# Performance work log

Hardware: AMD Instinct MI355X
Metric: run time of the kernel (lower is better)

Reference implementation:

```python
import jax, jax.numpy as jnp
import numpy as np

N1, N2, E = 256, 128, 4096

def _conv(x, w, b):
    # NCHW conv, 3x3, padding=1 (SAME), then ReLU
    y = jax.lax.conv_general_dilated(x, w, (1, 1), 'SAME',
                                     dimension_numbers=('NCHW', 'OIHW', 'NCHW'))
    return jax.nn.relu(y + b[None, :, None, None])

def _pool(x):
    return jax.lax.reduce_window(x, -jnp.inf, jax.lax.max,
                                 (1, 1, 2, 2), (1, 1, 2, 2), 'VALID')

def _sage(x, src, dst, wl, bl, wr, n):
    # torch_geometric SAGEConv: out = lin_l(mean_j x_src) + lin_r(x), then L2 normalize
    agg = jax.ops.segment_sum(x[src], dst, num_segments=n)
    cnt = jax.ops.segment_sum(jnp.ones((src.shape[0],), x.dtype), dst, num_segments=n)
    agg = agg / jnp.maximum(cnt, 1.0)[:, None]
    out = agg @ wl.T + bl + x @ wr.T
    return out / jnp.maximum(jnp.linalg.norm(out, axis=-1, keepdims=True), 1e-12)

def _diff_pool(x, adj, s):
    # torch_geometric dense_diff_pool
    s = jax.nn.softmax(s, axis=-1)
    out = jnp.einsum('bnc,bnf->bcf', s, x)
    out_adj = jnp.einsum('bnc,bnm,bmd->bcd', s, adj, s)
    link = adj - jnp.einsum('bnc,bmc->bnm', s, s)
    link_loss = jnp.sqrt(jnp.sum(link * link)) / adj.size
    ent_loss = jnp.mean(jnp.sum(-s * jnp.log(s + 1e-15), axis=-1))
    return out, out_adj, link_loss, ent_loss

def setup_inputs() -> dict:
    key = jax.random.key(0)
    ks = jax.random.split(key, 16)
    rn = lambda k, shape, sc: jax.random.normal(k, shape, jnp.float32) * sc
    inp = {}
    inp['inputs'] = jax.random.normal(ks[0], (1, 5, 512, 512), jnp.float32)
    inp['edge_index'] = jax.random.randint(ks[1], (2, E), 0, N1)
    chans = [(5, 32), (32, 64), (64, 128), (128, 256), (256, 256)]
    for i, (ci, co) in enumerate(chans):
        inp[f'w{i+1}'] = rn(ks[2 + i], (co, ci, 3, 3), 1.0 / np.sqrt(ci * 9))
        inp[f'b{i+1}'] = jnp.zeros((co,), jnp.float32)
    sdims = [(256, 128), (256, 128), (128, 2)]
    for i, (ci, co) in enumerate(sdims):
        inp[f'sage{i+1}_wl'] = rn(ks[7 + 2 * i], (co, ci), 1.0 / np.sqrt(ci))
        inp[f'sage{i+1}_bl'] = jnp.zeros((co,), jnp.float32)
        inp[f'sage{i+1}_wr'] = rn(ks[8 + 2 * i], (co, ci), 1.0 / np.sqrt(ci))
    return inp

def reference(inputs, edge_index, w1, b1, w2, b2, w3, b3, w4, b4, w5, b5,
              sage1_wl, sage1_bl, sage1_wr, sage2_wl, sage2_bl, sage2_wr,
              sage3_wl, sage3_bl, sage3_wr):
    x = _pool(_conv(inputs, w1, b1))
    x = _pool(_conv(x, w2, b2))
    x = _pool(_conv(x, w3, b3))
    x = _pool(_conv(x, w4, b4))
    x = _pool(_conv(x, w5, b5))            # [1,256,16,16]
    org = x.reshape(N1, N1)                # [256 nodes, 256 feats]
    src, dst = edge_index[0], edge_index[1]
    x1 = _sage(org, src, dst, sage1_wl, sage1_bl, sage1_wr, N1)
    s1 = _sage(org, src, dst, sage2_wl, sage2_bl, sage2_wr, N1)
    # dense adjacency (scipy coo->dense sums duplicate edges)
    adj1 = jnp.zeros((N1, N1), jnp.float32).at[src, dst].add(1.0)
    xp, adjp, ll1, el1 = _diff_pool(x1[None], adj1[None], s1[None])
    xp = xp.reshape(N2, N2)
    adjp = adjp.reshape(N2, N2)
    # vectorized form of the per-row in-place argmax binarization loop
    row_max = jnp.max(adjp, axis=1, keepdims=True)
    edge_out = jnp.where(adjp == row_max, 1.0, 0.0)
    # dense_to_sparse of the binarized matrix (one max per row, generic case)
    cols = jnp.argmax(adjp, axis=1)
    ei2 = jnp.stack([jnp.arange(N2), cols])  # [2,128] int
    nodes_out = jnp.tanh(_sage(xp, ei2[0], ei2[1], sage3_wl, sage3_bl, sage3_wr, N2))
    adj2 = jnp.zeros((N2, N2), jnp.float32).at[ei2[0], ei2[1]].add(1.0)
    s2 = jnp.ones((1, N2, 1), jnp.float32)  # softmax over size-1 dim -> ones
    x2, _, ll2, el2 = _diff_pool(nodes_out[None], adj2[None], s2)
    return (x2.reshape(-1), ll1 + ll2, el1 + el2, nodes_out, edge_out, ei2)
```

## Files before the change

### kernel.cpp

```cpp
#include <hip/hip_runtime.h>
#include <hip/hip_bf16.h>
#include <math.h>

#define N_EDGES 4096
#define NN1 256
#define NN2 128

typedef short v8s __attribute__((ext_vector_type(8)));
typedef float v4f __attribute__((ext_vector_type(4)));

__device__ inline unsigned short f2b(float f){
  union { __hip_bfloat16 h; unsigned short u; } cv;
  cv.h = __float2bfloat16(f);
  return cv.u;
}

template<int NT>
__device__ inline float block_sum(float v, float* red, int t){
  red[t] = v; __syncthreads();
  #pragma unroll
  for (int st = NT/2; st > 0; st >>= 1){
    if (t < st) red[t] += red[t+st];
    __syncthreads();
  }
  float r = red[0]; __syncthreads();
  return r;
}
template<int NT>
__device__ inline float block_max(float v, float* red, int t){
  red[t] = v; __syncthreads();
  #pragma unroll
  for (int st = NT/2; st > 0; st >>= 1){
    if (t < st) red[t] = fmaxf(red[t], red[t+st]);
    __syncthreads();
  }
  float r = red[0]; __syncthreads();
  return r;
}
template<int NT>
__device__ inline int block_min_int(int v, int* red, int t){
  red[t] = v; __syncthreads();
  #pragma unroll
  for (int st = NT/2; st > 0; st >>= 1){
    if (t < st) red[t] = min(red[t], red[t+st]);
    __syncthreads();
  }
  int r = red[0]; __syncthreads();
  return r;
}

template<int CHUNKS, int COUT, int CIN, int SSLABS, int BSTR, int OUTMODE>
__global__ __launch_bounds__(256) void conv_mfma(
    const unsigned short* __restrict__ in, const unsigned short* __restrict__ wb,
    const float* __restrict__ bias, unsigned short* __restrict__ outb,
    float* __restrict__ outf,
    int in_row, int in_slab, int out_row, int out_slab)
{
  constexpr int CG = COUT/32;
  __shared__ unsigned short tileb[SSLABS*2600];
  __shared__ unsigned short wldsb[9*32*40];

  const int cg = blockIdx.x % CG, bx = blockIdx.x / CG, by = blockIdx.y;
  const int z = blockIdx.z;
  const int cbase = z*CHUNKS;
  const int tid = threadIdx.x, lane = tid & 63, wv = tid >> 6;
  const int cot = wv >> 1, wp = wv & 1;
  const int ml = lane & 15, g = lane >> 4;

  v4f acc[8];
  #pragma unroll
  for (int t = 0; t < 8; ++t) acc[t] = (v4f){0.f,0.f,0.f,0.f};

  for (int cb = 0; cb < CHUNKS; ++cb){
    if (cb) __syncthreads();
    for (int j = tid; j < SSLABS*324; j += 256){
      int s = j / 324, rem = j - s*324;
      int row = rem / 18, px = rem - row*18;
      int gidx = ((cbase+cb)*SSLABS + s)*in_slab + ((by*16 + row)*in_row + bx*16 + px)*8;
      *(v8s*)&tileb[s*2600 + (row*18+px)*8] = *(const v8s*)&in[gidx];
    }
    for (int j = tid; j < 1152; j += 256){
      int k = j >> 7, rem = j & 127;
      int co = rem >> 2, q = rem & 3;
      int gw = (k*COUT + cg*32 + co)*CIN + (cbase+cb)*32 + q*8;
      *(v8s*)&wldsb[(k*32+co)*40 + q*8] = *(const v8s*)&wb[gw];
    }
    __syncthreads();

    #pragma unroll
    for (int k9 = 0; k9 < 9; ++k9){
      const int ky = k9/3, kx = k9 - 3*(k9/3);
      v8s a = *(const v8s*)&wldsb[(k9*32 + cot*16 + ml)*40 + g*8];
      #pragma unroll
      for (int tt = 0; tt < 8; ++tt){
        int t = wp*8 + tt;
        v8s b = *(const v8s*)&tileb[g*BSTR + ((t+ky)*18 + kx + ml)*8];
        acc[tt] = __builtin_amdgcn_mfma_f32_16x16x32_bf16(a, b, acc[tt], 0, 0, 0);
      }
    }
  }

  const int cob = cg*32 + cot*16 + g*4;
  if (OUTMODE == 2){
    const int W = out_row;
    #pragma unroll
    for (int tt = 0; tt < 8; ++tt){
      int gy = by*16 + wp*8 + tt, gx = bx*16 + ml;
      #pragma unroll
      for (int r = 0; r < 4; ++r)
        outf[((size_t)(z*COUT + cob + r)*W + gy)*W + gx] = acc[tt][r];
    }
    return;
  }

  float b4[4] = {bias[cob], bias[cob+1], bias[cob+2], bias[cob+3]};
  #pragma unroll
  for (int tp = 0; tp < 4; ++tp){
    float m[4];
    #pragma unroll
    for (int r = 0; r < 4; ++r){
      float v = fmaxf(acc[2*tp][r], acc[2*tp+1][r]);
      float o = __shfl_xor(v, 1);
      m[r] = fmaxf(fmaxf(v, o) + b4[r], 0.f);
    }
    if ((lane & 1) == 0){
      int gy = by*8 + wp*4 + tp, gx = bx*8 + (ml >> 1);
      if (OUTMODE == 1){
        #pragma unroll
        for (int r = 0; r < 4; ++r)
          outf[(cob + r)*256 + gy*16 + gx] = m[r];
      } else {
        unsigned int u0 = (unsigned)f2b(m[0]) | ((unsigned)f2b(m[1]) << 16);
        unsigned int u1 = (unsigned)f2b(m[2]) | ((unsigned)f2b(m[3]) << 16);
        int slabo = cob >> 3, sub = (g & 1)*4;
        size_t idx = (size_t)slabo*out_slab + (size_t)((gy+1)*out_row + gx+1)*8 + sub;
        *(uint2*)(outb + idx) = make_uint2(u0, u1);
      }
    }
  }
}

template<int SPLITK, int OUTF32>
__global__ __launch_bounds__(256) void reduce_pool(
    const float* __restrict__ pbuf, const float* __restrict__ bias,
    unsigned short* __restrict__ outb, float* __restrict__ outf,
    int COUT, int H, int W, int out_row, int out_slab)
{
  int idx = blockIdx.x*256 + threadIdx.x;
  const int OW = W >> 1, OH = H >> 1;
  if (idx >= COUT*OH*OW) return;
  int px = idx % OW; int t2 = idx / OW; int py = t2 % OH; int cout = t2 / OH;
  size_t base = ((size_t)cout*H + 2*py)*W + 2*px;
  size_t sstr = (size_t)COUT*H*W;
  float s00=0.f, s01=0.f, s10=0.f, s11=0.f;
  #pragma unroll
  for (int s = 0; s < SPLITK; ++s){
    const float* pb = pbuf + s*sstr + base;
    s00 += pb[0]; s01 += pb[1]; s10 += pb[W]; s11 += pb[W+1];
  }
  float m = fmaxf(fmaxf(fmaxf(s00,s01), fmaxf(s10,s11)) + bias[cout], 0.f);
  if (OUTF32){
    outf[cout*OH*OW + py*OW + px] = m;
  } else {
    outb[(size_t)(cout>>3)*out_slab + (size_t)((py+1)*out_row + px+1)*8 + (cout&7)] = f2b(m);
  }
}

__global__ __launch_bounds__(256) void prep_kernel(
    const float* __restrict__ src, unsigned short* __restrict__ p0b,
    const float* __restrict__ w1, const float* __restrict__ w2,
    const float* __restrict__ w3, const float* __restrict__ w4,
    const float* __restrict__ w5, unsigned short* __restrict__ wbb,
    const float* __restrict__ a, const float* __restrict__ b2,
    const float* __restrict__ c2, const float* __restrict__ d2,
    float* __restrict__ o, unsigned short* __restrict__ wsb,
    float* __restrict__ adjz)
{
  int b = blockIdx.x, tid = threadIdx.x;
  if (b < 1024){
    int idx = b*256 + tid;
    int y = idx >> 9, x = idx & 511;
    unsigned short v8[8];
    #pragma unroll
    for (int c = 0; c < 5; ++c) v8[c] = f2b(src[c*262144 + y*512 + x]);
    v8[5] = 0; v8[6] = 0; v8[7] = 0;
    *(uint4*)&p0b[((size_t)(y+1)*516 + (x+1))*8] = *(uint4*)v8;
  } else if (b < 1452){
    int j = (b-1024)*256 + tid;
    int co, ci, CO, CIl, CIsrc, dst; const float* w;
    if (j < 1024)      { co=j>>5;        ci=j&31;        w=w1; CIsrc=5;   CO=32;  CIl=32;  dst=0; }
    else if (j < 3072) { int q=j-1024;   co=q>>5;  ci=q&31;  w=w2; CIsrc=32;  CO=64;  CIl=32;  dst=9216; }
    else if (j < 11264){ int q=j-3072;   co=q>>6;  ci=q&63;  w=w3; CIsrc=64;  CO=128; CIl=64;  dst=27648; }
    else if (j < 44032){ int q=j-11264;  co=q>>7;  ci=q&127; w=w4; CIsrc=128; CO=256; CIl=128; dst=101376; }
    else               { int q=j-44032;  co=q>>8;  ci=q&255; w=w5; CIsrc=256; CO=256; CIl=256; dst=396288; }
    #pragma unroll
    for (int k = 0; k < 9; ++k){
      float val = (ci < CIsrc) ? w[(co*CIsrc + ci)*9 + k] : 0.f;
      wbb[dst + (k*CO + co)*CIl + ci] = f2b(val);
    }
  } else if (b < 1964){
    int idx = (b-1452)*256 + tid;
    int m = idx >> 15, rem = idx & 32767, k = rem >> 7, cc = rem & 127;
    const float* sp = (m==0)?a:(m==1)?b2:(m==2)?c2:d2;
    o[m*32768 + k*128 + cc] = sp[cc*256 + k];
  } else {
    int j = (b-1964)*256 + tid;
    const int c0=2056, c1=6184, c2z=10344, c3=14568, c4=18920, ca=35368;
    if (j >= ca) return;
    if (j >= c4){
      int q = j - c4;
      ((float4*)adjz)[q] = make_float4(0.f,0.f,0.f,0.f);
      return;
    }
    int base, P, R, W, per, rem;
    if (j < c0)       { base=0;       P=516; R=514; W=512; per=2056; rem=j; }
    else if (j < c1)  { base=2121792; P=260; R=258; W=256; per=1032; rem=j-c0; }
    else if (j < c2z) { base=4268352; P=132; R=130; W=128; per=520;  rem=j-c1; }
    else if (j < c3)  { base=5366592; P=68;  R=66;  W=64;  per=264;  rem=j-c2z; }
    else              { base=5941056; P=36;  R=34;  W=32;  per=136;  rem=j-c3; }
    int s = rem / per, r2 = rem - s*per;
    int row, px;
    if (r2 < 2*P){ row = (r2 < P) ? 0 : R-1; px = (r2 < P) ? r2 : r2 - P; }
    else { int q = r2 - 2*P; row = 1 + (q >> 1); px = (q & 1) ? (W+1) : 0; }
    *(uint4*)&wsb[(size_t)base + ((size_t)(s*R + row)*P + px)*8] = make_uint4(0,0,0,0);
  }
}

__global__ void build_adj_kernel(const int* __restrict__ ei, float* adj, float* cnt){
  int e = blockIdx.x*256 + threadIdx.x;
  if (e < N_EDGES){
    int s = ei[e], d = ei[N_EDGES + e];
    atomicAdd(&adj[s*NN1 + d], 1.0f);
    atomicAdd(&cnt[d], 1.0f);
  }
}

__global__ __launch_bounds__(128) void sage12_kernel(
    const float* __restrict__ adj, const float* __restrict__ cnt,
    const float* __restrict__ org,
    const float* __restrict__ wl1t, const float* __restrict__ bl1, const float* __restrict__ wr1t,
    const float* __restrict__ wl2t, const float* __restrict__ bl2, const float* __restrict__ wr2t,
    float* __restrict__ x1, float* __restrict__ s_out, float* __restrict__ st,
    float* __restrict__ entpart)
{
  __shared__ float sa[NN1], so[NN1], col[NN1], red[128];
  int n = blockIdx.x, c = threadIdx.x;
  for (int k = c; k < NN1; k += 128){
    col[k] = adj[k*NN1 + n];
    so[k]  = org[n*NN1 + k];
  }
  __syncthreads();
  float a0 = 0.f, a1 = 0.f;
  #pragma unroll 4
  for (int s2 = 0; s2 < NN1; ++s2){
    float av = col[s2];
    a0 += av * org[s2*NN1 + c];
    a1 += av * org[s2*NN1 + c + 128];
  }
  float cd = fmaxf(cnt[n], 1.0f);
  sa[c] = a0 / cd;
  sa[c+128] = a1 / cd;
  __syncthreads();

  float p1 = bl1[c], p2 = bl2[c];
  for (int k = 0; k < NN1; ++k){
    float av = sa[k], ov = so[k];
    p1 += av*wl1t[k*128+c] + ov*wr1t[k*128+c];
    p2 += av*wl2t[k*128+c] + ov*wr2t[k*128+c];
  }
  float n1s = block_sum<128>(p1*p1, red, c);
  x1[n*128 + c] = p1 / fmaxf(sqrtf(n1s), 1e-12f);
  float n2s = block_sum<128>(p2*p2, red, c);
  float p2n = p2 / fmaxf(sqrtf(n2s), 1e-12f);
  float mx = block_max<128>(p2n, red, c);
  float ev = expf(p2n - mx);
  float ssum = block_sum<128>(ev, red, c);
  float sv = ev / ssum;
  s_out[n*128 + c] = sv;
  st[c*NN1 + n] = sv;
  float esum = block_sum<128>(-sv * logf(sv + 1e-15f), red, c);
  if (c == 0) entpart[n] = esum;
}

__global__ __launch_bounds__(256) void fuse1_kernel(
    const float* __restrict__ s, const float* __restrict__ x1,
    const float* __restrict__ adj, const float* __restrict__ st,
    float* __restrict__ xp, float* __restrict__ t, float* __restrict__ linkpart)
{
  __shared__ float sn[128]; __shared__ float red[256];
  int b = blockIdx.x, tid = threadIdx.x;
  if (b < 64){
    int cc = b*2 + (tid >> 7), f = tid & 127;
    float acc = 0.f;
    for (int n = 0; n < NN1; ++n) acc += s[n*128+cc] * x1[n*128+f];
    xp[cc*128+f] = acc;
  } else if (b < 192){
    int n = (b-64)*2 + (tid >> 7), c = tid & 127;
    float acc = 0.f;
    for (int m = 0; m < NN1; ++m){
      float a = adj[n*NN1+m];
      if (a != 0.f) acc += a * s[m*128+c];
    }
    t[n*128+c] = acc;
  } else {
    int n = b - 192, m = tid;
    if (m < 128) sn[m] = s[n*128+m];
    __syncthreads();
    float dot = 0.f;
    for (int c = 0; c < 128; ++c) dot += sn[c]*st[c*NN1 + m];
    float v = adj[n*NN1+m] - dot;
    float part = block_sum<256>(v*v, red, m);
    if (m == 0) linkpart[n] = part;
  }
}

__global__ __launch_bounds__(128) void adjp_bin_kernel(
    const float* __restrict__ s, const float* __restrict__ t,
    float* __restrict__ edge_out, float* __restrict__ ei2_out, int* __restrict__ cols)
{
  __shared__ float scol[NN1]; __shared__ float red[128]; __shared__ int redi[128];
  int cc = blockIdx.x, j = threadIdx.x;
  scol[j]       = s[j*128 + cc];
  scol[j + 128] = s[(j+128)*128 + cc];
  __syncthreads();
  float acc = 0.f;
  for (int n = 0; n < NN1; ++n) acc += scol[n] * t[n*128 + j];
  float mx = block_max<128>(acc, red, j);
  edge_out[cc*128+j] = (acc == mx) ? 1.0f : 0.0f;
  int cand = (acc == mx) ? j : (1 << 30);
  int cmin = block_min_int<128>(cand, redi, j);
  if (j == 0){
    cols[cc] = cmin;
    ei2_out[cc] = (float)cc;
    ei2_out[128 + cc] = (float)cmin;
  }
}

__global__ __launch_bounds__(128) void sage3_kernel(
    const float* __restrict__ xp, const int* __restrict__ cols,
    const float* __restrict__ wl3, const float* __restrict__ bl3,
    const float* __restrict__ wr3, float* __restrict__ nodes_out)
{
  __shared__ int colsl[NN2]; __shared__ float red[128];
  int n = blockIdx.x, f = threadIdx.x;
  colsl[f] = cols[f];
  __syncthreads();
  float acc = 0.f, c = 0.f;
  for (int i = 0; i < NN2; ++i){
    if (colsl[i] == n){ acc += xp[i*128+f]; c += 1.f; }
  }
  float ag = acc / fmaxf(c, 1.f);
  float xv = xp[n*128+f];
  float q0 = block_sum<128>(ag*wl3[f]     + xv*wr3[f],     red, f);
  float q1 = block_sum<128>(ag*wl3[128+f] + xv*wr3[128+f], red, f);
  if (f == 0){
    float p0 = q0 + bl3[0], p1 = q1 + bl3[1];
    float nm = fmaxf(sqrtf(p0*p0 + p1*p1), 1e-12f);
    nodes_out[n*2+0] = tanhf(p0/nm);
    nodes_out[n*2+1] = tanhf(p1/nm);
  }
}

__global__ __launch_bounds__(256) void finalize_kernel(const float* __restrict__ linkpart,
    const float* __restrict__ entpart, float* __restrict__ d_out)
{
  __shared__ float red[256];
  int t = threadIdx.x;
  float ls = block_sum<256>(linkpart[t], red, t);
  float es = block_sum<256>(entpart[t], red, t);
  float v0 = 0.f, v1 = 0.f;
  if (t < 128){ v0 = d_out[4 + t*2 + 0]; v1 = d_out[4 + t*2 + 1]; }
  float s0 = block_sum<256>(v0, red, t);
  float s1 = block_sum<256>(v1, red, t);
  if (t == 0){
    d_out[0] = s0;
    d_out[1] = s1;
    d_out[2] = sqrtf(ls)/65536.0f + sqrtf(16256.0f)/16384.0f;
    d_out[3] = es/256.0f;
  }
}

extern "C" void kernel_launch(void* const* d_in, const int* in_sizes, int n_in,
                              void* d_out_v, int out_size, void* d_ws, size_t ws_size,
                              hipStream_t stream)
{
  (void)in_sizes; (void)n_in; (void)out_size; (void)ws_size;
  const float* input = (const float*)d_in[0];
  const int*   ei    = (const int*)  d_in[1];
  const float* w1 = (const float*)d_in[2];  const float* b1 = (const float*)d_in[3];
  const float* w2 = (const float*)d_in[4];  const float* b2 = (const float*)d_in[5];
  const float* w3 = (const float*)d_in[6];  const float* b3 = (const float*)d_in[7];
  const float* w4 = (const float*)d_in[8];  const float* b4 = (const float*)d_in[9];
  const float* w5 = (const float*)d_in[10]; const float* b5 = (const float*)d_in[11];
  const float* s1wl = (const float*)d_in[12]; const float* s1bl = (const float*)d_in[13];
  const float* s1wr = (const float*)d_in[14];
  const float* s2wl = (const float*)d_in[15]; const float* s2bl = (const float*)d_in[16];
  const float* s2wr = (const float*)d_in[17];
  const float* s3wl = (const float*)d_in[18]; const float* s3bl = (const float*)d_in[19];
  const float* s3wr = (const float*)d_in[20];
  float* d_out = (float*)d_out_v;
  float* ws = (float*)d_ws;

  unsigned short* P0b = (unsigned short*)(ws);
  unsigned short* Pb1 = (unsigned short*)(ws + 1060896);
  unsigned short* Pb2 = (unsigned short*)(ws + 2134176);
  unsigned short* Pb3 = (unsigned short*)(ws + 2683296);
  unsigned short* Pb4 = (unsigned short*)(ws + 2970528);
  unsigned short* wb  = (unsigned short*)(ws + 3127200);
  float* org = ws + 3620256;
  float* wt  = ws + 3685792;
  float* st  = ws + 3816864;
  float* G   = ws + 3849632;

  float* adj1     = G;
  float* cnt      = G + 65536;
  float* x1       = G + 147712;
  float* s        = G + 180480;
  float* t        = G + 213248;
  float* xp       = G + 246016;
  int*   cols     = (int*)(G + 278784);
  float* linkpart = G + 278912;
  float* entpart  = G + 279168;
  float* PART     = ws + 4129280;

  prep_kernel<<<dim3(2103), 256, 0, stream>>>(input, P0b, w1, w2, w3, w4, w5, wb,
                                              s1wl, s1wr, s2wl, s2wr, wt,
                                              (unsigned short*)ws, adj1);

  conv_mfma<1,32,32,1,0,0>      <<<dim3(32,32),   256, 0, stream>>>(P0b, wb,        b1, Pb1, nullptr, 516, 2121792, 260, 536640);
  conv_mfma<1,64,32,4,2600,0>   <<<dim3(32,16),   256, 0, stream>>>(Pb1, wb+9216,   b2, Pb2, nullptr, 260, 536640, 132, 137280);
  conv_mfma<2,128,64,4,2600,0>  <<<dim3(32,8),    256, 0, stream>>>(Pb2, wb+27648,  b3, Pb3, nullptr, 132, 137280, 68,  35904);
  conv_mfma<2,256,128,4,2600,2> <<<dim3(32,4,2),  256, 0, stream>>>(Pb3, wb+101376, b4, nullptr, PART, 68, 35904, 64, 0);
  reduce_pool<2,0>              <<<dim3(1024),    256, 0, stream>>>(PART, b4, Pb4, nullptr, 256, 64, 64, 36, 9792);
  conv_mfma<1,256,256,4,2600,2> <<<dim3(16,2,8),  256, 0, stream>>>(Pb4, wb+396288, b5, nullptr, PART, 36, 9792, 32, 0);
  reduce_pool<8,1>              <<<dim3(256),     256, 0, stream>>>(PART, b5, nullptr, org, 256, 32, 32, 0, 0);

  build_adj_kernel<<<dim3(16),  256, 0, stream>>>(ei, adj1, cnt);
  sage12_kernel   <<<dim3(256), 128, 0, stream>>>(adj1, cnt, org, wt, s1bl, wt+32768,
                                                  wt+65536, s2bl, wt+98304, x1, s, st, entpart);
  fuse1_kernel    <<<dim3(448), 256, 0, stream>>>(s, x1, adj1, st, xp, t, linkpart);
  adjp_bin_kernel <<<dim3(128), 128, 0, stream>>>(s, t, d_out + 260, d_out + 16644, cols);
  sage3_kernel    <<<dim3(128), 128, 0, stream>>>(xp, cols, s3wl, s3bl, s3wr, d_out + 4);
  finalize_kernel <<<dim3(1),   256, 0, stream>>>(linkpart, entpart, d_out);
}
```

Before: 178.7 us.

## Fuse edge scatter into final pool reduce and widen small graph kernels

Folds the adjacency/count atomic scatter into the last split-K reduce+pool kernel as extra blocks, which removes one launch. sage12 moves to 256 threads: each thread does one aggregation column, and each half of the block computes one of the two SAGE projections. adjp_bin splits its 256-long dot product across two thread halves. The aim is to cut launch count and raise thread-level parallelism in the latency-bound tail kernels, at the cost of extra reductions over half-idle lanes.

```diff
diff --git a/kernel.cpp b/kernel.cpp
--- a/kernel.cpp
+++ b/kernel.cpp
@@ -140,11 +140,11 @@
   }
 }
 
-template<int SPLITK, int OUTF32>
-__global__ __launch_bounds__(256) void reduce_pool(
+template<int SPLITK>
+__global__ __launch_bounds__(256) void reduce_pool_b(
     const float* __restrict__ pbuf, const float* __restrict__ bias,
-    unsigned short* __restrict__ outb, float* __restrict__ outf,
-    int COUT, int H, int W, int out_row, int out_slab)
+    unsigned short* __restrict__ outb, int COUT, int H, int W,
+    int out_row, int out_slab)
 {
   int idx = blockIdx.x*256 + threadIdx.x;
   const int OW = W >> 1, OH = H >> 1;
@@ -159,10 +159,36 @@
     s00 += pb[0]; s01 += pb[1]; s10 += pb[W]; s11 += pb[W+1];
   }
   float m = fmaxf(fmaxf(fmaxf(s00,s01), fmaxf(s10,s11)) + bias[cout], 0.f);
-  if (OUTF32){
+  outb[(size_t)(cout>>3)*out_slab + (size_t)((py+1)*out_row + px+1)*8 + (cout&7)] = f2b(m);
+}
+
+__global__ __launch_bounds__(256) void reduce5_adj_kernel(
+    const float* __restrict__ pbuf, const float* __restrict__ bias,
+    float* __restrict__ outf, const int* __restrict__ ei,
+    float* __restrict__ adj, float* __restrict__ cnt)
+{
+  int b = blockIdx.x;
+  if (b < 256){
+    int idx = b*256 + threadIdx.x;
+    const int OW=16, OH=16, W=32, H=32, COUT=256;
+    int px = idx % OW; int t2 = idx / OW; int py = t2 % OH; int cout = t2 / OH;
+    size_t base = ((size_t)cout*H + 2*py)*W + 2*px;
+    size_t sstr = (size_t)COUT*H*W;
+    float s00=0.f, s01=0.f, s10=0.f, s11=0.f;
+    #pragma unroll
+    for (int s = 0; s < 8; ++s){
+      const float* pb = pbuf + s*sstr + base;
+      s00 += pb[0]; s01 += pb[1]; s10 += pb[W]; s11 += pb[W+1];
+    }
+    float m = fmaxf(fmaxf(fmaxf(s00,s01), fmaxf(s10,s11)) + bias[cout], 0.f);
     outf[cout*OH*OW + py*OW + px] = m;
   } else {
-    outb[(size_t)(cout>>3)*out_slab + (size_t)((py+1)*out_row + px+1)*8 + (cout&7)] = f2b(m);
+    int e = (b-256)*256 + threadIdx.x;
+    if (e < N_EDGES){
+      int sn = ei[e], dn = ei[N_EDGES + e];
+      atomicAdd(&adj[sn*NN1 + dn], 1.0f);
+      atomicAdd(&cnt[dn], 1.0f);
+    }
   }
 }
 
@@ -226,16 +252,7 @@
   }
 }
 
-__global__ void build_adj_kernel(const int* __restrict__ ei, float* adj, float* cnt){
-  int e = blockIdx.x*256 + threadIdx.x;
-  if (e < N_EDGES){
-    int s = ei[e], d = ei[N_EDGES + e];
-    atomicAdd(&adj[s*NN1 + d], 1.0f);
-    atomicAdd(&cnt[d], 1.0f);
-  }
-}
-
-__global__ __launch_bounds__(128) void sage12_kernel(
+__global__ __launch_bounds__(256) void sage12_kernel(
     const float* __restrict__ adj, const float* __restrict__ cnt,
     const float* __restrict__ org,
     const float* __restrict__ wl1t, const float* __restrict__ bl1, const float* __restrict__ wr1t,
@@ -243,43 +260,39 @@
     float* __restrict__ x1, float* __restrict__ s_out, float* __restrict__ st,
     float* __restrict__ entpart)
 {
-  __shared__ float sa[NN1], so[NN1], col[NN1], red[128];
-  int n = blockIdx.x, c = threadIdx.x;
-  for (int k = c; k < NN1; k += 128){
-    col[k] = adj[k*NN1 + n];
-    so[k]  = org[n*NN1 + k];
-  }
+  __shared__ float sa[NN1], so[NN1], col[NN1], red[256];
+  int n = blockIdx.x, tid = threadIdx.x;
+  col[tid] = adj[tid*NN1 + n];
+  so[tid]  = org[n*NN1 + tid];
   __syncthreads();
-  float a0 = 0.f, a1 = 0.f;
+  float a0 = 0.f;
   #pragma unroll 4
-  for (int s2 = 0; s2 < NN1; ++s2){
-    float av = col[s2];
-    a0 += av * org[s2*NN1 + c];
-    a1 += av * org[s2*NN1 + c + 128];
-  }
-  float cd = fmaxf(cnt[n], 1.0f);
-  sa[c] = a0 / cd;
-  sa[c+128] = a1 / cd;
+  for (int s2 = 0; s2 < NN1; ++s2) a0 += col[s2] * org[s2*NN1 + tid];
+  sa[tid] = a0 / fmaxf(cnt[n], 1.0f);
   __syncthreads();
 
-  float p1 = bl1[c], p2 = bl2[c];
-  for (int k = 0; k < NN1; ++k){
-    float av = sa[k], ov = so[k];
-    p1 += av*wl1t[k*128+c] + ov*wr1t[k*128+c];
-    p2 += av*wl2t[k*128+c] + ov*wr2t[k*128+c];
-  }
-  float n1s = block_sum<128>(p1*p1, red, c);
-  x1[n*128 + c] = p1 / fmaxf(sqrtf(n1s), 1e-12f);
-  float n2s = block_sum<128>(p2*p2, red, c);
-  float p2n = p2 / fmaxf(sqrtf(n2s), 1e-12f);
-  float mx = block_max<128>(p2n, red, c);
+  const int c = tid & 127;
+  const bool lo = tid < 128;
+  const float* wlt = lo ? wl1t : wl2t;
+  const float* wrt = lo ? wr1t : wr2t;
+  float p = lo ? bl1[c] : bl2[c];
+  for (int k = 0; k < NN1; ++k)
+    p += sa[k]*wlt[k*128+c] + so[k]*wrt[k*128+c];
+
+  float n1s = block_sum<256>(lo ? p*p : 0.f, red, tid);
+  if (lo) x1[n*128 + c] = p / fmaxf(sqrtf(n1s), 1e-12f);
+  float n2s = block_sum<256>(lo ? 0.f : p*p, red, tid);
+  float p2n = p / fmaxf(sqrtf(n2s), 1e-12f);
+  float mx = block_max<256>(lo ? -INFINITY : p2n, red, tid);
   float ev = expf(p2n - mx);
-  float ssum = block_sum<128>(ev, red, c);
+  float ssum = block_sum<256>(lo ? 0.f : ev, red, tid);
   float sv = ev / ssum;
-  s_out[n*128 + c] = sv;
-  st[c*NN1 + n] = sv;
-  float esum = block_sum<128>(-sv * logf(sv + 1e-15f), red, c);
-  if (c == 0) entpart[n] = esum;
+  if (!lo){
+    s_out[n*128 + c] = sv;
+    st[c*NN1 + n] = sv;
+  }
+  float esum = block_sum<256>(lo ? 0.f : (-sv * logf(sv + 1e-15f)), red, tid);
+  if (tid == 0) entpart[n] = esum;
 }
 
 __global__ __launch_bounds__(256) void fuse1_kernel(
@@ -314,22 +327,25 @@
   }
 }
 
-__global__ __launch_bounds__(128) void adjp_bin_kernel(
+__global__ __launch_bounds__(256) void adjp_bin_kernel(
     const float* __restrict__ s, const float* __restrict__ t,
     float* __restrict__ edge_out, float* __restrict__ ei2_out, int* __restrict__ cols)
 {
-  __shared__ float scol[NN1]; __shared__ float red[128]; __shared__ int redi[128];
-  int cc = blockIdx.x, j = threadIdx.x;
-  scol[j]       = s[j*128 + cc];
-  scol[j + 128] = s[(j+128)*128 + cc];
+  __shared__ float scol[NN1]; __shared__ float red[256]; __shared__ int redi[256];
+  int cc = blockIdx.x, tid = threadIdx.x;
+  int j = tid & 127, h = tid >> 7;
+  scol[tid] = s[tid*128 + cc];
   __syncthreads();
-  float acc = 0.f;
-  for (int n = 0; n < NN1; ++n) acc += scol[n] * t[n*128 + j];
-  float mx = block_max<128>(acc, red, j);
-  edge_out[cc*128+j] = (acc == mx) ? 1.0f : 0.0f;
+  float part = 0.f;
+  for (int n = h*128; n < (h+1)*128; ++n) part += scol[n] * t[n*128 + j];
+  red[tid] = part; __syncthreads();
+  float acc = red[j] + red[j+128];
+  __syncthreads();
+  float mx = block_max<256>(acc, red, tid);
+  if (h == 0) edge_out[cc*128+j] = (acc == mx) ? 1.0f : 0.0f;
   int cand = (acc == mx) ? j : (1 << 30);
-  int cmin = block_min_int<128>(cand, redi, j);
-  if (j == 0){
+  int cmin = block_min_int<256>(cand, redi, tid);
+  if (tid == 0){
     cols[cc] = cmin;
     ei2_out[cc] = (float)cc;
     ei2_out[128 + cc] = (float)cmin;
@@ -431,15 +447,14 @@
   conv_mfma<1,64,32,4,2600,0>   <<<dim3(32,16),   256, 0, stream>>>(Pb1, wb+9216,   b2, Pb2, nullptr, 260, 536640, 132, 137280);
   conv_mfma<2,128,64,4,2600,0>  <<<dim3(32,8),    256, 0, stream>>>(Pb2, wb+27648,  b3, Pb3, nullptr, 132, 137280, 68,  35904);
   conv_mfma<2,256,128,4,2600,2> <<<dim3(32,4,2),  256, 0, stream>>>(Pb3, wb+101376, b4, nullptr, PART, 68, 35904, 64, 0);
-  reduce_pool<2,0>              <<<dim3(1024),    256, 0, stream>>>(PART, b4, Pb4, nullptr, 256, 64, 64, 36, 9792);
+  reduce_pool_b<2>              <<<dim3(1024),    256, 0, stream>>>(PART, b4, Pb4, 256, 64, 64, 36, 9792);
   conv_mfma<1,256,256,4,2600,2> <<<dim3(16,2,8),  256, 0, stream>>>(Pb4, wb+396288, b5, nullptr, PART, 36, 9792, 32, 0);
-  reduce_pool<8,1>              <<<dim3(256),     256, 0, stream>>>(PART, b5, nullptr, org, 256, 32, 32, 0, 0);
-
-  build_adj_kernel<<<dim3(16),  256, 0, stream>>>(ei, adj1, cnt);
-  sage12_kernel   <<<dim3(256), 128, 0, stream>>>(adj1, cnt, org, wt, s1bl, wt+32768,
+  reduce5_adj_kernel            <<<dim3(272),     256, 0, stream>>>(PART, b5, org, ei, adj1, cnt);
+
+  sage12_kernel   <<<dim3(256), 256, 0, stream>>>(adj1, cnt, org, wt, s1bl, wt+32768,
                                                   wt+65536, s2bl, wt+98304, x1, s, st, entpart);
   fuse1_kernel    <<<dim3(448), 256, 0, stream>>>(s, x1, adj1, st, xp, t, linkpart);
-  adjp_bin_kernel <<<dim3(128), 128, 0, stream>>>(s, t, d_out + 260, d_out + 16644, cols);
+  adjp_bin_kernel <<<dim3(128), 256, 0, stream>>>(s, t, d_out + 260, d_out + 16644, cols);
   sage3_kernel    <<<dim3(128), 128, 0, stream>>>(xp, cols, s3wl, s3bl, s3wr, d_out + 4);
   finalize_kernel <<<dim3(1),   256, 0, stream>>>(linkpart, entpart, d_out);
 }
```

Result: slower. 200.0 us (+11.9%).
